# Kernel optimization log

Measured on AMD Instinct MI355X. Metric: run time of the kernel, lower is better.

## Reference

```python
import jax, jax.numpy as jnp
import numpy as np

K = 128          # num_clusters (init kwarg k)
N_ITERS = 100    # torch loop runs up to 100 iters; converged centroids are a
                 # fixed point, so running all 100 matches the early-exit result


def _sq_dists(x, c):
    # squared Euclidean distances [N, K]; argmin identical to torch.cdist argmin
    return (jnp.sum(x * x, axis=1, keepdims=True)
            - 2.0 * (x @ c.T)
            + jnp.sum(c * c, axis=1)[None, :])


def _assign_and_update(x, c):
    ids = jnp.argmin(_sq_dists(x, c), axis=1)                     # [N]
    sums = jax.ops.segment_sum(x, ids, num_segments=K)            # [K, D]
    counts = jax.ops.segment_sum(jnp.ones((x.shape[0],), x.dtype), ids,
                                 num_segments=K)                  # [K]
    return ids, sums / counts[:, None]   # mean per cluster (NaN if empty, as in torch)


def setup_inputs() -> dict:
    key = jax.random.key(0)
    kx, kp = jax.random.split(key)
    N, D = 32768, 256
    x = jax.random.normal(kx, (N, D), dtype=jnp.float32)
    # torch.randperm(N)[:K] -> distinct initial centroid indices
    init_idx = jax.random.permutation(kp, N)[:K].astype(jnp.int32)
    return {"x": x, "init_idx": init_idx}


def reference(x, init_idx):
    c0 = x[init_idx]  # [K, D]

    def body(c, _):
        _, newc = _assign_and_update(x, c)
        return newc, None

    # 99 updates, then final assignment + update: returned ids correspond to the
    # centroids BEFORE the last update, exactly like the torch loop's last iter.
    c, _ = jax.lax.scan(body, c0, None, length=N_ITERS - 1)
    ids, c = _assign_and_update(x, c)

    logits = x @ c.T  # temperature = 1.0
    logp = jax.nn.log_softmax(logits, axis=-1)
    # CrossEntropyLoss(mean) with pseudo labels = cluster ids
    loss = -jnp.mean(jnp.take_along_axis(logp, ids[:, None], axis=1))
    return loss
```

## Files before the change

### kernel.cpp

```cpp
#include <hip/hip_runtime.h>
#include <cstdint>

#define NPTS 32768
#define DIM  256
#define NK   128
#define NITER 100

typedef __attribute__((ext_vector_type(8))) short s8v;
typedef __attribute__((ext_vector_type(4))) float f4v;

__device__ __forceinline__ unsigned short f2bf(float f) {
  unsigned u = __float_as_uint(f);
  u += 0x7fffu + ((u >> 16) & 1u);
  return (unsigned short)(u >> 16);
}
__device__ __forceinline__ float bf2f(unsigned short b) {
  return __uint_as_float(((unsigned)b) << 16);
}

__global__ __launch_bounds__(256) void prep_x_kernel(const float* __restrict__ x,
    unsigned short* __restrict__ xh, unsigned short* __restrict__ xl) {
  for (int i = 0; i < 16; ++i) {
    int g = blockIdx.x * 4096 + i * 256 + threadIdx.x;
    const float4* src = (const float4*)x + g * 2;
    float4 a = src[0], b = src[1];
    float vv[8] = {a.x, a.y, a.z, a.w, b.x, b.y, b.z, b.w};
    s8v vh, vl;
#pragma unroll
    for (int j = 0; j < 8; ++j) {
      unsigned short h = f2bf(vv[j]);
      vh[j] = (short)h;
      vl[j] = (short)f2bf(vv[j] - bf2f(h));
    }
    ((s8v*)xh)[g] = vh;
    ((s8v*)xl)[g] = vl;
  }
}

__global__ void init_c_kernel(const float* __restrict__ x, const int* __restrict__ idx,
                              unsigned short* __restrict__ chi, unsigned short* __restrict__ clo,
                              float* __restrict__ cn) {
  int k = blockIdx.x, d = threadIdx.x;
  float v = x[idx[k] * DIM + d];
  unsigned short h = f2bf(v);
  unsigned short l = f2bf(v - bf2f(h));
  chi[k * DIM + d] = h;
  clo[k * DIM + d] = l;
  float eff = bf2f(h) + bf2f(l);
  __shared__ float red[256];
  red[d] = eff * eff;
  __syncthreads();
  for (int s = 128; s > 0; s >>= 1) { if (d < s) red[d] += red[d + s]; __syncthreads(); }
  if (d == 0) cn[k] = red[0];
}

template <int MODE>
__global__ __launch_bounds__(256) void gemm_epi_kernel(
    const unsigned short* __restrict__ xh, const unsigned short* __restrict__ xl,
    const unsigned short* __restrict__ chi, const unsigned short* __restrict__ clo,
    const float* __restrict__ cn, int* __restrict__ ids, float* __restrict__ out) {
  __shared__ s8v bufs[4][2048];
  __shared__ float cns[NK];
  __shared__ float redd[NK * 2];
  __shared__ int   redk[NK * 2];
  __shared__ float gmaxs[NK];
  __shared__ float labvs[NK];
  __shared__ int   labis[NK];

  const int t    = threadIdx.x;
  const int lane = t & 63;
  const int w    = t >> 6;
  const int wr   = w >> 1, wc = w & 1;
  const int g    = lane >> 4, lr = lane & 15;
  const int pbase = blockIdx.x * 128;

  if (t < NK) cns[t] = cn[t];

  f4v acc[4][4];
  const f4v zero = {0.f, 0.f, 0.f, 0.f};
#pragma unroll
  for (int i = 0; i < 4; ++i)
#pragma unroll
    for (int j = 0; j < 4; ++j) acc[i][j] = zero;

  const int swz = (lr & 7) << 4;
  int a_off[4], b_off[4];
#pragma unroll
  for (int i = 0; i < 4; ++i) a_off[i] = (wr * 64 + i * 16 + lr) * 256 + g * 16;
#pragma unroll
  for (int j = 0; j < 4; ++j) b_off[j] = (wc * 64 + j * 16 + lr) * 256 + g * 16;

  const unsigned short* srcs[4];
  srcs[0] = xh + pbase * DIM;
  srcs[1] = xl + pbase * DIM;
  srcs[2] = chi;
  srcs[3] = clo;

  for (int h = 0; h < 2; ++h) {
    __syncthreads();
#pragma unroll
    for (int b = 0; b < 4; ++b) {
      const char* sp = (const char*)srcs[b];
      char* dp = (char*)bufs[b];
#pragma unroll
      for (int i = 0; i < 8; ++i) {
        int gg = i * 256 + t;
        int row = gg >> 4, whb = (gg & 15) * 16;
        s8v v = *(const s8v*)(sp + row * 512 + h * 256 + whb);
        *(s8v*)(dp + ((gg * 16) ^ ((row & 7) << 4))) = v;
      }
    }
    __syncthreads();
#pragma unroll
    for (int kk = 0; kk < 4; ++kk) {
      s8v ah[4], al[4], bh[4], bl[4];
#pragma unroll
      for (int i = 0; i < 4; ++i) {
        int o = (a_off[i] + kk * 64) ^ swz;
        ah[i] = *(const s8v*)((const char*)bufs[0] + o);
        al[i] = *(const s8v*)((const char*)bufs[1] + o);
      }
#pragma unroll
      for (int j = 0; j < 4; ++j) {
        int o = (b_off[j] + kk * 64) ^ swz;
        bh[j] = *(const s8v*)((const char*)bufs[2] + o);
        bl[j] = *(const s8v*)((const char*)bufs[3] + o);
      }
#pragma unroll
      for (int i = 0; i < 4; ++i)
#pragma unroll
        for (int j = 0; j < 4; ++j) {
          acc[i][j] = __builtin_amdgcn_mfma_f32_16x16x32_bf16(ah[i], bh[j], acc[i][j], 0, 0, 0);
          acc[i][j] = __builtin_amdgcn_mfma_f32_16x16x32_bf16(ah[i], bl[j], acc[i][j], 0, 0, 0);
          acc[i][j] = __builtin_amdgcn_mfma_f32_16x16x32_bf16(al[i], bh[j], acc[i][j], 0, 0, 0);
        }
    }
  }

  if (MODE == 0) {
#pragma unroll
    for (int i = 0; i < 4; ++i) {
#pragma unroll
      for (int r = 0; r < 4; ++r) {
        int prow = wr * 64 + i * 16 + g * 4 + r;
        float bd = 1e30f; int bk = 0;
#pragma unroll
        for (int j = 0; j < 4; ++j) {
          int col = wc * 64 + j * 16 + lr;
          float s = cns[col] - 2.f * acc[i][j][r];
          if (s < bd || (s == bd && col < bk)) { bd = s; bk = col; }
        }
#pragma unroll
        for (int msk = 1; msk < 16; msk <<= 1) {
          float od = __shfl_xor(bd, msk, 64);
          int   ok = __shfl_xor(bk, msk, 64);
          if (od < bd || (od == bd && ok < bk)) { bd = od; bk = ok; }
        }
        if (lr == 0) { redd[prow * 2 + wc] = bd; redk[prow * 2 + wc] = bk; }
      }
    }
    __syncthreads();
    if (t < NK) {
      float d0 = redd[t * 2], d1 = redd[t * 2 + 1];
      int k0 = redk[t * 2], k1 = redk[t * 2 + 1];
      ids[pbase + t] = (d1 < d0 || (d1 == d0 && k1 < k0)) ? k1 : k0;
    }
  }

  if (MODE == 1) {
#pragma unroll
    for (int i = 0; i < 4; ++i) {
#pragma unroll
      for (int r = 0; r < 4; ++r) {
        int prow = wr * 64 + i * 16 + g * 4 + r;
        float m = -1e30f;
#pragma unroll
        for (int j = 0; j < 4; ++j) m = fmaxf(m, acc[i][j][r]);
#pragma unroll
        for (int msk = 1; msk < 16; msk <<= 1) m = fmaxf(m, __shfl_xor(m, msk, 64));
        if (lr == 0) redd[prow * 2 + wc] = m;
      }
    }
    __syncthreads();
    if (t < NK) {
      gmaxs[t] = fmaxf(redd[t * 2], redd[t * 2 + 1]);
      labis[t] = ids[pbase + t];
    }
    __syncthreads();
#pragma unroll
    for (int i = 0; i < 4; ++i) {
#pragma unroll
      for (int r = 0; r < 4; ++r) {
        int prow = wr * 64 + i * 16 + g * 4 + r;
        float m = gmaxs[prow];
        int lab = labis[prow];
        float s = 0.f;
#pragma unroll
        for (int j = 0; j < 4; ++j) {
          int col = wc * 64 + j * 16 + lr;
          float v = acc[i][j][r];
          s += expf(v - m);
          if (col == lab) labvs[prow] = v;
        }
#pragma unroll
        for (int msk = 1; msk < 16; msk <<= 1) s += __shfl_xor(s, msk, 64);
        if (lr == 0) redd[prow * 2 + wc] = s;
      }
    }
    __syncthreads();
    if (t < NK) {
      float se  = redd[t * 2] + redd[t * 2 + 1];
      float lse = gmaxs[t] + logf(se);
      gmaxs[t] = lse - labvs[t];
    }
    __syncthreads();
    if (t == 0) {
      float tot = 0.f;
      for (int q = 0; q < NK; ++q) tot += gmaxs[q];
      atomicAdd(out, tot * (1.0f / (float)NPTS));
    }
  }
}

__global__ __launch_bounds__(256) void update_partial_kernel(
    const float* __restrict__ x, const int* __restrict__ ids,
    float* __restrict__ psum, float* __restrict__ pcnt) {
  __shared__ float ls[NK * 32];
  __shared__ float lc[NK];
  __shared__ int idsl[1024];
  const int t = threadIdx.x;
  const int pc = blockIdx.x & 31, dc = blockIdx.x >> 5;
  for (int r = t; r < NK * 32; r += 256) ls[r] = 0.f;
  if (t < NK) lc[t] = 0.f;
  for (int r = t; r < 1024; r += 256) idsl[r] = ids[pc * 1024 + r];
  __syncthreads();
  const int sub = t >> 5, dl = t & 31;
  const int dcol = dc * 32 + dl;
  for (int s = 0; s < 128; ++s) {
    int pl = s * 8 + sub;
    int id = idsl[pl];
    float v = x[(pc * 1024 + pl) * DIM + dcol];
    atomicAdd(&ls[id * 32 + dl], v);
    if (dc == 0 && dl == 0) atomicAdd(&lc[id], 1.f);
  }
  __syncthreads();
  for (int r = 0; r < 16; ++r) {
    int idx = r * 256 + t;
    int k = idx >> 5, d2 = idx & 31;
    psum[(pc * NK + k) * DIM + dc * 32 + d2] = ls[k * 32 + d2];
  }
  if (dc == 0 && t < NK) pcnt[pc * NK + t] = lc[t];
}

__global__ void reduce_update_kernel(const float* __restrict__ psum, const float* __restrict__ pcnt,
                                     unsigned short* __restrict__ chi, unsigned short* __restrict__ clo,
                                     float* __restrict__ cn) {
  int k = blockIdx.x, d = threadIdx.x;
  float s = 0.f;
  for (int pc = 0; pc < 32; ++pc) s += psum[(pc * NK + k) * DIM + d];
  float cntv = 0.f;
  for (int pc = 0; pc < 32; ++pc) cntv += pcnt[pc * NK + k];
  float mean = s / cntv;
  unsigned short h = f2bf(mean);
  unsigned short l = f2bf(mean - bf2f(h));
  chi[k * DIM + d] = h;
  clo[k * DIM + d] = l;
  float eff = bf2f(h) + bf2f(l);
  __shared__ float red[256];
  red[d] = eff * eff;
  __syncthreads();
  for (int st = 128; st > 0; st >>= 1) { if (d < st) red[d] += red[d + st]; __syncthreads(); }
  if (d == 0) cn[k] = red[0];
}

extern "C" void kernel_launch(void* const* d_in, const int* in_sizes, int n_in,
                              void* d_out, int out_size, void* d_ws, size_t ws_size,
                              hipStream_t stream) {
  const float* x        = (const float*)d_in[0];
  const int*   init_idx = (const int*)d_in[1];
  float* out = (float*)d_out;
  char* ws = (char*)d_ws;

  unsigned short* xh  = (unsigned short*)(ws);
  unsigned short* xl  = (unsigned short*)(ws + 16777216);
  unsigned short* chi = (unsigned short*)(ws + 33554432);
  unsigned short* clo = (unsigned short*)(ws + 33619968);
  float* cn   = (float*)(ws + 33685504);
  int*   ids  = (int*)(ws + 33686016);
  float* psum = (float*)(ws + 33817088);
  float* pcnt = (float*)(ws + 38011392);

  hipMemsetAsync(out, 0, sizeof(float), stream);
  prep_x_kernel<<<256, 256, 0, stream>>>(x, xh, xl);
  init_c_kernel<<<NK, 256, 0, stream>>>(x, init_idx, chi, clo, cn);
  for (int it = 0; it < NITER; ++it) {
    gemm_epi_kernel<0><<<NPTS / 128, 256, 0, stream>>>(xh, xl, chi, clo, cn, ids, out);
    update_partial_kernel<<<256, 256, 0, stream>>>(x, ids, psum, pcnt);
    reduce_update_kernel<<<NK, 256, 0, stream>>>(psum, pcnt, chi, clo, cn);
  }
  gemm_epi_kernel<1><<<NPTS / 128, 256, 0, stream>>>(xh, xl, chi, clo, cn, ids, out);
}
```

Before: 8.280 ms.

## Fuse all k-means stages into one persistent kernel with grid barriers

Replaces the roughly 300 separate kernel launches (GEMM/assign, partial update, reduce per iteration) with a single persistent kernel of 256 blocks that synchronises between phases through a software grid barrier on global atomics. Shared memory is overlaid with a union across phases, and the final loss is reduced deterministically per block instead of with a global atomic. This removes per-launch overhead and the gaps between launches. It relies on all 256 blocks being resident at once, since the barrier would deadlock otherwise, and each barrier adds spin-wait cost.

```diff
diff --git a/kernel.cpp b/kernel.cpp
--- a/kernel.cpp
+++ b/kernel.cpp
@@ -5,6 +5,7 @@
 #define DIM  256
 #define NK   128
 #define NITER 100
+#define NBLK 256
 
 typedef __attribute__((ext_vector_type(8))) short s8v;
 typedef __attribute__((ext_vector_type(4))) float f4v;
@@ -18,65 +19,58 @@
   return __uint_as_float(((unsigned)b) << 16);
 }
 
-__global__ __launch_bounds__(256) void prep_x_kernel(const float* __restrict__ x,
-    unsigned short* __restrict__ xh, unsigned short* __restrict__ xl) {
-  for (int i = 0; i < 16; ++i) {
-    int g = blockIdx.x * 4096 + i * 256 + threadIdx.x;
-    const float4* src = (const float4*)x + g * 2;
-    float4 a = src[0], b = src[1];
-    float vv[8] = {a.x, a.y, a.z, a.w, b.x, b.y, b.z, b.w};
-    s8v vh, vl;
-#pragma unroll
-    for (int j = 0; j < 8; ++j) {
-      unsigned short h = f2bf(vv[j]);
-      vh[j] = (short)h;
-      vl[j] = (short)f2bf(vv[j] - bf2f(h));
-    }
-    ((s8v*)xh)[g] = vh;
-    ((s8v*)xl)[g] = vl;
-  }
-}
-
-__global__ void init_c_kernel(const float* __restrict__ x, const int* __restrict__ idx,
-                              unsigned short* __restrict__ chi, unsigned short* __restrict__ clo,
-                              float* __restrict__ cn) {
-  int k = blockIdx.x, d = threadIdx.x;
-  float v = x[idx[k] * DIM + d];
-  unsigned short h = f2bf(v);
-  unsigned short l = f2bf(v - bf2f(h));
-  chi[k * DIM + d] = h;
-  clo[k * DIM + d] = l;
-  float eff = bf2f(h) + bf2f(l);
-  __shared__ float red[256];
-  red[d] = eff * eff;
+__device__ __forceinline__ void gbar(unsigned* bar) {
   __syncthreads();
-  for (int s = 128; s > 0; s >>= 1) { if (d < s) red[d] += red[d + s]; __syncthreads(); }
-  if (d == 0) cn[k] = red[0];
-}
-
-template <int MODE>
-__global__ __launch_bounds__(256) void gemm_epi_kernel(
+  if (threadIdx.x == 0) {
+    __threadfence();
+    unsigned g = __hip_atomic_load(&bar[1], __ATOMIC_RELAXED, __HIP_MEMORY_SCOPE_AGENT);
+    unsigned a = __hip_atomic_fetch_add(&bar[0], 1u, __ATOMIC_ACQ_REL, __HIP_MEMORY_SCOPE_AGENT);
+    if (a == (unsigned)NBLK - 1u) {
+      __hip_atomic_store(&bar[0], 0u, __ATOMIC_RELAXED, __HIP_MEMORY_SCOPE_AGENT);
+      __hip_atomic_store(&bar[1], g + 1u, __ATOMIC_RELEASE, __HIP_MEMORY_SCOPE_AGENT);
+    } else {
+      while (__hip_atomic_load(&bar[1], __ATOMIC_RELAXED, __HIP_MEMORY_SCOPE_AGENT) == g) {
+        __builtin_amdgcn_s_sleep(2);
+      }
+    }
+    __threadfence();
+  }
+  __syncthreads();
+}
+
+union SMu {
+  struct {
+    s8v bufs[4][2048];
+    float cns[NK];
+    float redd[NK * 2];
+    int   redk[NK * 2];
+    float gmaxs[NK];
+    float labvs[NK];
+    int   labis[NK];
+  } a;
+  struct {
+    float ls[NK * 32];
+    float lc[NK];
+    int   idsl[1024];
+  } b;
+  struct {
+    float red[256];
+  } c;
+};
+
+__device__ __forceinline__ void gemm_core(
+    SMu& sm, int b, int t,
     const unsigned short* __restrict__ xh, const unsigned short* __restrict__ xl,
     const unsigned short* __restrict__ chi, const unsigned short* __restrict__ clo,
-    const float* __restrict__ cn, int* __restrict__ ids, float* __restrict__ out) {
-  __shared__ s8v bufs[4][2048];
-  __shared__ float cns[NK];
-  __shared__ float redd[NK * 2];
-  __shared__ int   redk[NK * 2];
-  __shared__ float gmaxs[NK];
-  __shared__ float labvs[NK];
-  __shared__ int   labis[NK];
-
-  const int t    = threadIdx.x;
+    const float* __restrict__ cn, f4v (&acc)[4][4]) {
   const int lane = t & 63;
   const int w    = t >> 6;
   const int wr   = w >> 1, wc = w & 1;
   const int g    = lane >> 4, lr = lane & 15;
-  const int pbase = blockIdx.x * 128;
-
-  if (t < NK) cns[t] = cn[t];
-
-  f4v acc[4][4];
+  const int pbase = b * 128;
+
+  if (t < NK) sm.a.cns[t] = cn[t];
+
   const f4v zero = {0.f, 0.f, 0.f, 0.f};
 #pragma unroll
   for (int i = 0; i < 4; ++i)
@@ -99,9 +93,9 @@
   for (int h = 0; h < 2; ++h) {
     __syncthreads();
 #pragma unroll
-    for (int b = 0; b < 4; ++b) {
-      const char* sp = (const char*)srcs[b];
-      char* dp = (char*)bufs[b];
+    for (int bb = 0; bb < 4; ++bb) {
+      const char* sp = (const char*)srcs[bb];
+      char* dp = (char*)sm.a.bufs[bb];
 #pragma unroll
       for (int i = 0; i < 8; ++i) {
         int gg = i * 256 + t;
@@ -117,14 +111,14 @@
 #pragma unroll
       for (int i = 0; i < 4; ++i) {
         int o = (a_off[i] + kk * 64) ^ swz;
-        ah[i] = *(const s8v*)((const char*)bufs[0] + o);
-        al[i] = *(const s8v*)((const char*)bufs[1] + o);
+        ah[i] = *(const s8v*)((const char*)sm.a.bufs[0] + o);
+        al[i] = *(const s8v*)((const char*)sm.a.bufs[1] + o);
       }
 #pragma unroll
       for (int j = 0; j < 4; ++j) {
         int o = (b_off[j] + kk * 64) ^ swz;
-        bh[j] = *(const s8v*)((const char*)bufs[2] + o);
-        bl[j] = *(const s8v*)((const char*)bufs[3] + o);
+        bh[j] = *(const s8v*)((const char*)sm.a.bufs[2] + o);
+        bl[j] = *(const s8v*)((const char*)sm.a.bufs[3] + o);
       }
 #pragma unroll
       for (int i = 0; i < 4; ++i)
@@ -136,38 +130,137 @@
         }
     }
   }
-
-  if (MODE == 0) {
-#pragma unroll
-    for (int i = 0; i < 4; ++i) {
-#pragma unroll
-      for (int r = 0; r < 4; ++r) {
-        int prow = wr * 64 + i * 16 + g * 4 + r;
-        float bd = 1e30f; int bk = 0;
-#pragma unroll
-        for (int j = 0; j < 4; ++j) {
-          int col = wc * 64 + j * 16 + lr;
-          float s = cns[col] - 2.f * acc[i][j][r];
-          if (s < bd || (s == bd && col < bk)) { bd = s; bk = col; }
+}
+
+__global__ __launch_bounds__(256, 1) void kmeans_fused(
+    const float* __restrict__ x, const int* __restrict__ init_idx,
+    unsigned short* __restrict__ xh, unsigned short* __restrict__ xl,
+    unsigned short* __restrict__ chi, unsigned short* __restrict__ clo,
+    float* __restrict__ cn, int* __restrict__ ids,
+    float* __restrict__ psum, float* __restrict__ pcnt,
+    float* __restrict__ outp, unsigned* __restrict__ bar,
+    float* __restrict__ out) {
+  __shared__ SMu sm;
+
+  const int b = blockIdx.x;
+  const int t = threadIdx.x;
+  const int lane = t & 63;
+  const int w  = t >> 6;
+  const int wr = w >> 1, wc = w & 1;
+  const int g  = lane >> 4, lr = lane & 15;
+  const int pbase = b * 128;
+
+  for (int i = 0; i < 16; ++i) {
+    int gg = b * 4096 + i * 256 + t;
+    const float4* src = (const float4*)x + gg * 2;
+    float4 fa = src[0], fb = src[1];
+    float vv[8] = {fa.x, fa.y, fa.z, fa.w, fb.x, fb.y, fb.z, fb.w};
+    s8v vh, vl;
+#pragma unroll
+    for (int j = 0; j < 8; ++j) {
+      unsigned short hh = f2bf(vv[j]);
+      vh[j] = (short)hh;
+      vl[j] = (short)f2bf(vv[j] - bf2f(hh));
+    }
+    ((s8v*)xh)[gg] = vh;
+    ((s8v*)xl)[gg] = vl;
+  }
+
+  if (b < NK) {
+    float v = x[init_idx[b] * DIM + t];
+    unsigned short hh = f2bf(v);
+    unsigned short ll = f2bf(v - bf2f(hh));
+    chi[b * DIM + t] = hh;
+    clo[b * DIM + t] = ll;
+    float eff = bf2f(hh) + bf2f(ll);
+    sm.c.red[t] = eff * eff;
+    __syncthreads();
+    for (int s = 128; s > 0; s >>= 1) { if (t < s) sm.c.red[t] += sm.c.red[t + s]; __syncthreads(); }
+    if (t == 0) cn[b] = sm.c.red[0];
+  }
+  gbar(bar);
+
+  for (int it = 0; it < NITER; ++it) {
+    {
+      f4v acc[4][4];
+      gemm_core(sm, b, t, xh, xl, chi, clo, cn, acc);
+#pragma unroll
+      for (int i = 0; i < 4; ++i) {
+#pragma unroll
+        for (int r = 0; r < 4; ++r) {
+          int prow = wr * 64 + i * 16 + g * 4 + r;
+          float bd = 1e30f; int bk = 0;
+#pragma unroll
+          for (int j = 0; j < 4; ++j) {
+            int col = wc * 64 + j * 16 + lr;
+            float s = sm.a.cns[col] - 2.f * acc[i][j][r];
+            if (s < bd || (s == bd && col < bk)) { bd = s; bk = col; }
+          }
+#pragma unroll
+          for (int msk = 1; msk < 16; msk <<= 1) {
+            float od = __shfl_xor(bd, msk, 64);
+            int   ok = __shfl_xor(bk, msk, 64);
+            if (od < bd || (od == bd && ok < bk)) { bd = od; bk = ok; }
+          }
+          if (lr == 0) { sm.a.redd[prow * 2 + wc] = bd; sm.a.redk[prow * 2 + wc] = bk; }
         }
-#pragma unroll
-        for (int msk = 1; msk < 16; msk <<= 1) {
-          float od = __shfl_xor(bd, msk, 64);
-          int   ok = __shfl_xor(bk, msk, 64);
-          if (od < bd || (od == bd && ok < bk)) { bd = od; bk = ok; }
-        }
-        if (lr == 0) { redd[prow * 2 + wc] = bd; redk[prow * 2 + wc] = bk; }
-      }
-    }
-    __syncthreads();
-    if (t < NK) {
-      float d0 = redd[t * 2], d1 = redd[t * 2 + 1];
-      int k0 = redk[t * 2], k1 = redk[t * 2 + 1];
-      ids[pbase + t] = (d1 < d0 || (d1 == d0 && k1 < k0)) ? k1 : k0;
-    }
-  }
-
-  if (MODE == 1) {
+      }
+      __syncthreads();
+      if (t < NK) {
+        float d0 = sm.a.redd[t * 2], d1 = sm.a.redd[t * 2 + 1];
+        int k0 = sm.a.redk[t * 2], k1 = sm.a.redk[t * 2 + 1];
+        ids[pbase + t] = (d1 < d0 || (d1 == d0 && k1 < k0)) ? k1 : k0;
+      }
+    }
+    gbar(bar);
+
+    {
+      const int pc = b & 31, dc = b >> 5;
+      for (int r = t; r < NK * 32; r += 256) sm.b.ls[r] = 0.f;
+      if (t < NK) sm.b.lc[t] = 0.f;
+      for (int r = t; r < 1024; r += 256) sm.b.idsl[r] = ids[pc * 1024 + r];
+      __syncthreads();
+      const int sub = t >> 5, dl = t & 31;
+      const int dcol = dc * 32 + dl;
+      for (int s = 0; s < 128; ++s) {
+        int pl = s * 8 + sub;
+        int id = sm.b.idsl[pl];
+        float v = x[(pc * 1024 + pl) * DIM + dcol];
+        atomicAdd(&sm.b.ls[id * 32 + dl], v);
+        if (dc == 0 && dl == 0) atomicAdd(&sm.b.lc[id], 1.f);
+      }
+      __syncthreads();
+      for (int r = 0; r < 16; ++r) {
+        int idx = r * 256 + t;
+        int k = idx >> 5, d2 = idx & 31;
+        psum[(pc * NK + k) * DIM + dc * 32 + d2] = sm.b.ls[k * 32 + d2];
+      }
+      if (dc == 0 && t < NK) pcnt[pc * NK + t] = sm.b.lc[t];
+    }
+    gbar(bar);
+
+    if (b < NK) {
+      float s = 0.f;
+      for (int pc = 0; pc < 32; ++pc) s += psum[(pc * NK + b) * DIM + t];
+      float cntv = 0.f;
+      for (int pc = 0; pc < 32; ++pc) cntv += pcnt[pc * NK + b];
+      float mean = s / cntv;
+      unsigned short hh = f2bf(mean);
+      unsigned short ll = f2bf(mean - bf2f(hh));
+      chi[b * DIM + t] = hh;
+      clo[b * DIM + t] = ll;
+      float eff = bf2f(hh) + bf2f(ll);
+      sm.c.red[t] = eff * eff;
+      __syncthreads();
+      for (int st = 128; st > 0; st >>= 1) { if (t < st) sm.c.red[t] += sm.c.red[t + st]; __syncthreads(); }
+      if (t == 0) cn[b] = sm.c.red[0];
+    }
+    gbar(bar);
+  }
+
+  {
+    f4v acc[4][4];
+    gemm_core(sm, b, t, xh, xl, chi, clo, cn, acc);
 #pragma unroll
     for (int i = 0; i < 4; ++i) {
 #pragma unroll
@@ -178,13 +271,13 @@
         for (int j = 0; j < 4; ++j) m = fmaxf(m, acc[i][j][r]);
 #pragma unroll
         for (int msk = 1; msk < 16; msk <<= 1) m = fmaxf(m, __shfl_xor(m, msk, 64));
-        if (lr == 0) redd[prow * 2 + wc] = m;
+        if (lr == 0) sm.a.redd[prow * 2 + wc] = m;
       }
     }
     __syncthreads();
     if (t < NK) {
-      gmaxs[t] = fmaxf(redd[t * 2], redd[t * 2 + 1]);
-      labis[t] = ids[pbase + t];
+      sm.a.gmaxs[t] = fmaxf(sm.a.redd[t * 2], sm.a.redd[t * 2 + 1]);
+      sm.a.labis[t] = ids[pbase + t];
     }
     __syncthreads();
 #pragma unroll
@@ -192,85 +285,41 @@
 #pragma unroll
       for (int r = 0; r < 4; ++r) {
         int prow = wr * 64 + i * 16 + g * 4 + r;
-        float m = gmaxs[prow];
-        int lab = labis[prow];
+        float m = sm.a.gmaxs[prow];
+        int lab = sm.a.labis[prow];
         float s = 0.f;
 #pragma unroll
         for (int j = 0; j < 4; ++j) {
           int col = wc * 64 + j * 16 + lr;
           float v = acc[i][j][r];
           s += expf(v - m);
-          if (col == lab) labvs[prow] = v;
+          if (col == lab) sm.a.labvs[prow] = v;
         }
 #pragma unroll
         for (int msk = 1; msk < 16; msk <<= 1) s += __shfl_xor(s, msk, 64);
-        if (lr == 0) redd[prow * 2 + wc] = s;
+        if (lr == 0) sm.a.redd[prow * 2 + wc] = s;
       }
     }
     __syncthreads();
     if (t < NK) {
-      float se  = redd[t * 2] + redd[t * 2 + 1];
-      float lse = gmaxs[t] + logf(se);
-      gmaxs[t] = lse - labvs[t];
+      float se  = sm.a.redd[t * 2] + sm.a.redd[t * 2 + 1];
+      float lse = sm.a.gmaxs[t] + logf(se);
+      sm.a.gmaxs[t] = lse - sm.a.labvs[t];
     }
     __syncthreads();
     if (t == 0) {
       float tot = 0.f;
-      for (int q = 0; q < NK; ++q) tot += gmaxs[q];
-      atomicAdd(out, tot * (1.0f / (float)NPTS));
-    }
-  }
-}
-
-__global__ __launch_bounds__(256) void update_partial_kernel(
-    const float* __restrict__ x, const int* __restrict__ ids,
-    float* __restrict__ psum, float* __restrict__ pcnt) {
-  __shared__ float ls[NK * 32];
-  __shared__ float lc[NK];
-  __shared__ int idsl[1024];
-  const int t = threadIdx.x;
-  const int pc = blockIdx.x & 31, dc = blockIdx.x >> 5;
-  for (int r = t; r < NK * 32; r += 256) ls[r] = 0.f;
-  if (t < NK) lc[t] = 0.f;
-  for (int r = t; r < 1024; r += 256) idsl[r] = ids[pc * 1024 + r];
-  __syncthreads();
-  const int sub = t >> 5, dl = t & 31;
-  const int dcol = dc * 32 + dl;
-  for (int s = 0; s < 128; ++s) {
-    int pl = s * 8 + sub;
-    int id = idsl[pl];
-    float v = x[(pc * 1024 + pl) * DIM + dcol];
-    atomicAdd(&ls[id * 32 + dl], v);
-    if (dc == 0 && dl == 0) atomicAdd(&lc[id], 1.f);
-  }
-  __syncthreads();
-  for (int r = 0; r < 16; ++r) {
-    int idx = r * 256 + t;
-    int k = idx >> 5, d2 = idx & 31;
-    psum[(pc * NK + k) * DIM + dc * 32 + d2] = ls[k * 32 + d2];
-  }
-  if (dc == 0 && t < NK) pcnt[pc * NK + t] = lc[t];
-}
-
-__global__ void reduce_update_kernel(const float* __restrict__ psum, const float* __restrict__ pcnt,
-                                     unsigned short* __restrict__ chi, unsigned short* __restrict__ clo,
-                                     float* __restrict__ cn) {
-  int k = blockIdx.x, d = threadIdx.x;
-  float s = 0.f;
-  for (int pc = 0; pc < 32; ++pc) s += psum[(pc * NK + k) * DIM + d];
-  float cntv = 0.f;
-  for (int pc = 0; pc < 32; ++pc) cntv += pcnt[pc * NK + k];
-  float mean = s / cntv;
-  unsigned short h = f2bf(mean);
-  unsigned short l = f2bf(mean - bf2f(h));
-  chi[k * DIM + d] = h;
-  clo[k * DIM + d] = l;
-  float eff = bf2f(h) + bf2f(l);
-  __shared__ float red[256];
-  red[d] = eff * eff;
-  __syncthreads();
-  for (int st = 128; st > 0; st >>= 1) { if (d < st) red[d] += red[d + st]; __syncthreads(); }
-  if (d == 0) cn[k] = red[0];
+      for (int q = 0; q < NK; ++q) tot += sm.a.gmaxs[q];
+      outp[b] = tot;
+    }
+  }
+  gbar(bar);
+  if (b == 0) {
+    sm.c.red[t] = outp[t];
+    __syncthreads();
+    for (int s = 128; s > 0; s >>= 1) { if (t < s) sm.c.red[t] += sm.c.red[t + s]; __syncthreads(); }
+    if (t == 0) out[0] = sm.c.red[0] * (1.0f / (float)NPTS);
+  }
 }
 
 extern "C" void kernel_launch(void* const* d_in, const int* in_sizes, int n_in,
@@ -289,14 +338,10 @@
   int*   ids  = (int*)(ws + 33686016);
   float* psum = (float*)(ws + 33817088);
   float* pcnt = (float*)(ws + 38011392);
-
-  hipMemsetAsync(out, 0, sizeof(float), stream);
-  prep_x_kernel<<<256, 256, 0, stream>>>(x, xh, xl);
-  init_c_kernel<<<NK, 256, 0, stream>>>(x, init_idx, chi, clo, cn);
-  for (int it = 0; it < NITER; ++it) {
-    gemm_epi_kernel<0><<<NPTS / 128, 256, 0, stream>>>(xh, xl, chi, clo, cn, ids, out);
-    update_partial_kernel<<<256, 256, 0, stream>>>(x, ids, psum, pcnt);
-    reduce_update_kernel<<<NK, 256, 0, stream>>>(psum, pcnt, chi, clo, cn);
-  }
-  gemm_epi_kernel<1><<<NPTS / 128, 256, 0, stream>>>(xh, xl, chi, clo, cn, ids, out);
-}
+  float* outp = (float*)(ws + 38027776);
+  unsigned* bar = (unsigned*)(ws + 38028800);
+
+  hipMemsetAsync(bar, 0, 256, stream);
+  kmeans_fused<<<dim3(NBLK), dim3(256), 0, stream>>>(
+      x, init_idx, xh, xl, chi, clo, cn, ids, psum, pcnt, outp, bar, out);
+}
```

After: 16.21 ms. 1.96x slower.
